# Optimization experiments

Hardware: AMD Instinct MI355X
Metric: run time of the kernel (lower is better)

The kernel has to match this reference:

```python
import jax, jax.numpy as jnp
import numpy as np

B, T, C, H = 4, 2048, 1024, 16
D = C // H  # head_dim = 64
ROPE_BASE = 10000.0
EPS = 1e-6


def _rms_norm(x):
    return x / jnp.sqrt(jnp.mean(x * x, axis=-1, keepdims=True) + EPS)


def _rope_tables(t_len, d, dtype):
    inv_freq = 1.0 / (ROPE_BASE ** (jnp.arange(0, d, 2, dtype=jnp.float32) / d))
    t = jnp.arange(t_len, dtype=jnp.float32)
    freqs = jnp.outer(t, inv_freq)  # [T, D/2]
    return jnp.cos(freqs).astype(dtype)[None, None], jnp.sin(freqs).astype(dtype)[None, None]


def _apply_rotary(x, cos, sin):
    d = x.shape[-1] // 2
    x1, x2 = x[..., :d], x[..., d:]
    return jnp.concatenate([x1 * cos + x2 * sin, -x1 * sin + x2 * cos], axis=-1)


def setup_inputs() -> dict:
    key = jax.random.key(0)
    k1, k2, k3, k4, k5 = jax.random.split(key, 5)
    x = jax.random.normal(k1, (B, T, C), dtype=jnp.float32)
    Wqkv = jax.random.normal(k2, (C, 3 * C), dtype=jnp.float32) * 0.02
    bqkv = jax.random.normal(k3, (3 * C,), dtype=jnp.float32) * 0.02
    # NOTE: original zero-inits c_proj.weight; randomized here for a non-trivial baseline.
    Wproj = jax.random.normal(k4, (C, C), dtype=jnp.float32) * 0.02
    bproj = jax.random.normal(k5, (C,), dtype=jnp.float32) * 0.02
    lamb = jnp.float32(0.5)
    return {"x": x, "Wqkv": Wqkv, "bqkv": bqkv, "Wproj": Wproj, "bproj": bproj, "lamb": lamb}


def reference(x, Wqkv, bqkv, Wproj, bproj, lamb):
    b, t, c = x.shape
    qkv = x @ Wqkv + bqkv  # [B,T,3C]
    q, k, v = jnp.split(qkv, 3, axis=-1)
    # [B,T,C] -> [B,H,T,D]
    to_heads = lambda z: z.reshape(b, t, H, D).transpose(0, 2, 1, 3)
    query, key_, value = to_heads(q), to_heads(k), to_heads(v)
    # v1 defaults to value -> blend is identity, kept for faithfulness
    value = (1.0 - lamb) * value + lamb * value
    query = _rms_norm(query)
    key_ = _rms_norm(key_)
    cos, sin = _rope_tables(t, D, x.dtype)
    query = _apply_rotary(query, cos, sin)
    key_ = _apply_rotary(key_, cos, sin)
    # causal SDPA
    scale = 1.0 / jnp.sqrt(jnp.float32(D)).astype(x.dtype)
    scores = jnp.einsum('bhqd,bhkd->bhqk', query, key_) * scale
    causal = jnp.tril(jnp.ones((t, t), dtype=bool))
    scores = jnp.where(causal[None, None], scores, jnp.finfo(scores.dtype).min)
    probs = jax.nn.softmax(scores, axis=-1)
    attn = jnp.einsum('bhqk,bhkd->bhqd', probs, value)
    attn = attn.transpose(0, 2, 1, 3).reshape(b, t, c)
    out = attn @ Wproj + bproj
    return out, value
```

## Files before the change

### kernel.cpp

```cpp
#include <hip/hip_runtime.h>
#include <math.h>

#define B_   4
#define T_   2048
#define C_   1024
#define H_   16
#define D_   64
#define TC3  3072

typedef __attribute__((ext_vector_type(8))) short short8;
typedef __attribute__((ext_vector_type(4))) short short4b;
typedef __attribute__((ext_vector_type(8))) unsigned short ushortv8;
typedef __attribute__((ext_vector_type(4))) float f32x4;
typedef __attribute__((ext_vector_type(4))) __bf16 bf16x4;

__device__ __forceinline__ float bf2f(unsigned short u) {
  unsigned int x = ((unsigned int)u) << 16;
  float f; __builtin_memcpy(&f, &x, 4); return f;
}
__device__ __forceinline__ unsigned short f2bf(float f) {
  unsigned int x; __builtin_memcpy(&x, &f, 4);
  x += 0x7fff + ((x >> 16) & 1);
  return (unsigned short)(x >> 16);
}

#define MFMA32(a, b, c) __builtin_amdgcn_mfma_f32_16x16x32_bf16(a, b, c, 0, 0, 0)
#if __has_builtin(__builtin_amdgcn_mfma_f32_16x16x16_bf16)
#define MFMA16(a, b, c) __builtin_amdgcn_mfma_f32_16x16x16_bf16(a, b, c, 0, 0, 0)
#else
#define MFMA16(a, b, c) __builtin_amdgcn_mfma_f32_16x16x16bf16_1k(a, b, c, 0, 0, 0)
#endif

#define GLOAD_LDS(gp, lp) __builtin_amdgcn_global_load_lds( \
    (const __attribute__((address_space(1))) unsigned int*)(gp), \
    (__attribute__((address_space(3))) unsigned int*)(lp), 16, 0, 0)

__global__ __launch_bounds__(256)
void convert_bf16(const float* __restrict__ x, unsigned short* __restrict__ xb) {
  const size_t i = ((size_t)blockIdx.x * 256 + threadIdx.x) * 8;
  float4 f0 = *(const float4*)(x + i);
  float4 f1 = *(const float4*)(x + i + 4);
  ushortv8 u = { f2bf(f0.x), f2bf(f0.y), f2bf(f0.z), f2bf(f0.w),
                 f2bf(f1.x), f2bf(f1.y), f2bf(f1.z), f2bf(f1.w) };
  *(ushortv8*)(xb + i) = u;
}

__global__ __launch_bounds__(256)
void transpose_bf16(const float* __restrict__ W, unsigned short* __restrict__ WT,
                    int K, int N) {
  __shared__ float tile[64][65];
  const int k0 = blockIdx.y * 64, n0 = blockIdx.x * 64;
  const int r = threadIdx.x >> 4, c4 = (threadIdx.x & 15) * 4;
#pragma unroll
  for (int p = 0; p < 4; ++p) {
    int kk = p * 16 + r;
    float4 v = *(const float4*)(W + (size_t)(k0 + kk) * N + n0 + c4);
    tile[kk][c4 + 0] = v.x; tile[kk][c4 + 1] = v.y;
    tile[kk][c4 + 2] = v.z; tile[kk][c4 + 3] = v.w;
  }
  __syncthreads();
#pragma unroll
  for (int p = 0; p < 4; ++p) {
    int nn = p * 16 + r;
    ushort4 o = { f2bf(tile[c4 + 0][nn]), f2bf(tile[c4 + 1][nn]),
                  f2bf(tile[c4 + 2][nn]), f2bf(tile[c4 + 3][nn]) };
    *(ushort4*)(WT + (size_t)(n0 + nn) * K + k0 + c4) = o;
  }
}

template<bool OUT_BF16>
__global__ __launch_bounds__(256)
void gemm_mfma(const unsigned short* __restrict__ Ab,
               const unsigned short* __restrict__ Bt,
               const float* __restrict__ bias, void* __restrict__ Cv,
               int K, int lda, int ldb, int ldc) {
  __shared__ unsigned short As[128 * 64];
  __shared__ unsigned short Bs[128 * 64];
  const int tid = threadIdx.x;
  const int l = tid & 63, w = tid >> 6;
  const int m0 = blockIdx.y * 128, n0 = blockIdx.x * 128;
  const int wm = (w & 1) * 64, wn = (w >> 1) * 64;
  const int fr = l & 15, g = l >> 4;

  f32x4 acc[4][4];
#pragma unroll
  for (int i = 0; i < 4; ++i)
#pragma unroll
    for (int j = 0; j < 4; ++j) acc[i][j] = (f32x4)0.f;

  const int gr = l >> 3;
  const int gc = (l & 7) ^ gr;

  for (int kt = 0; kt < K; kt += 64) {
    __syncthreads();
#pragma unroll
    for (int q = 0; q < 4; ++q) {
      int rr = (w * 4 + q) * 8 + gr;
      GLOAD_LDS(Ab + (size_t)(m0 + rr) * lda + kt + gc * 8,
                &As[(w * 4 + q) * 512]);
      GLOAD_LDS(Bt + (size_t)(n0 + rr) * ldb + kt + gc * 8,
                &Bs[(w * 4 + q) * 512]);
    }
    __syncthreads();

#pragma unroll
    for (int s = 0; s < 2; ++s) {
      const int cofs = (((s * 4 + g) ^ (fr & 7)) << 3);
      short8 a[4], b[4];
#pragma unroll
      for (int i = 0; i < 4; ++i)
        a[i] = *(const short8*)&As[(wm + i * 16 + fr) * 64 + cofs];
#pragma unroll
      for (int j = 0; j < 4; ++j)
        b[j] = *(const short8*)&Bs[(wn + j * 16 + fr) * 64 + cofs];
#pragma unroll
      for (int i = 0; i < 4; ++i)
#pragma unroll
        for (int j = 0; j < 4; ++j)
          acc[i][j] = MFMA32(a[i], b[j], acc[i][j]);
    }
  }

#pragma unroll
  for (int j = 0; j < 4; ++j) {
    const int n = n0 + wn + j * 16 + fr;
    const float bv = bias[n];
#pragma unroll
    for (int i = 0; i < 4; ++i) {
#pragma unroll
      for (int rg = 0; rg < 4; ++rg) {
        const int m = m0 + wm + i * 16 + g * 4 + rg;
        float v = acc[i][j][rg] + bv;
        if (OUT_BF16) ((unsigned short*)Cv)[(size_t)m * ldc + n] = f2bf(v);
        else          ((float*)Cv)[(size_t)m * ldc + n] = v;
      }
    }
  }
}

__global__ __launch_bounds__(256)
void rmsrope_kernel(unsigned short* __restrict__ qkv) {
  const int unit = blockIdx.x * 4 + (threadIdx.x >> 6);
  const int lane = threadIdx.x & 63;
  const int b = unit / (T_ * H_);
  const int rem = unit % (T_ * H_);
  const int t = rem / H_;
  const int h = rem % H_;
  const size_t base = (size_t)(b * T_ + t) * TC3;

  const int i = lane & 31;
  const float inv = __builtin_amdgcn_exp2f(-13.2877123795494f * (float)(2 * i)
                                           * (1.0f / 64.0f));
  const float ang = (float)t * inv;
  const float cs = cosf(ang);
  const float sn = sinf(ang);

  {
    const size_t idx = base + h * 64 + lane;
    float q = bf2f(qkv[idx]);
    float ss = q * q;
    ss += __shfl_xor(ss, 32); ss += __shfl_xor(ss, 16);
    ss += __shfl_xor(ss, 8);  ss += __shfl_xor(ss, 4);
    ss += __shfl_xor(ss, 2);  ss += __shfl_xor(ss, 1);
    float qn = q * (1.0f / sqrtf(ss * (1.0f / 64.0f) + 1e-6f));
    float part = __shfl_xor(qn, 32);
    float out = (lane < 32) ? (qn * cs + part * sn) : (qn * cs - part * sn);
    qkv[idx] = f2bf(out);
  }
  {
    const size_t idx = base + C_ + h * 64 + lane;
    float k = bf2f(qkv[idx]);
    float ss = k * k;
    ss += __shfl_xor(ss, 32); ss += __shfl_xor(ss, 16);
    ss += __shfl_xor(ss, 8);  ss += __shfl_xor(ss, 4);
    ss += __shfl_xor(ss, 2);  ss += __shfl_xor(ss, 1);
    float kn = k * (1.0f / sqrtf(ss * (1.0f / 64.0f) + 1e-6f));
    float part = __shfl_xor(kn, 32);
    float out = (lane < 32) ? (kn * cs + part * sn) : (kn * cs - part * sn);
    qkv[idx] = f2bf(out);
  }
}

__global__ __launch_bounds__(256)
void vtrans_kernel(const unsigned short* __restrict__ qkv,
                   const float* __restrict__ lambp,
                   unsigned short* __restrict__ vT,
                   float* __restrict__ valOut) {
  __shared__ float tile[64][65];
  const int t0 = blockIdx.x * 64;
  const int head = blockIdx.y;
  const int b = head >> 4, h = head & 15;
  const float lamb = lambp[0];
  const int r = threadIdx.x >> 4, c4 = (threadIdx.x & 15) * 4;
#pragma unroll
  for (int p = 0; p < 4; ++p) {
    int tt = p * 16 + r;
    ushort4 raw = *(const ushort4*)(
        qkv + (size_t)(b * T_ + t0 + tt) * TC3 + 2 * C_ + h * 64 + c4);
    float4 f;
    f.x = (1.f - lamb) * bf2f(raw.x) + lamb * bf2f(raw.x);
    f.y = (1.f - lamb) * bf2f(raw.y) + lamb * bf2f(raw.y);
    f.z = (1.f - lamb) * bf2f(raw.z) + lamb * bf2f(raw.z);
    f.w = (1.f - lamb) * bf2f(raw.w) + lamb * bf2f(raw.w);
    tile[tt][c4 + 0] = f.x; tile[tt][c4 + 1] = f.y;
    tile[tt][c4 + 2] = f.z; tile[tt][c4 + 3] = f.w;
    *(float4*)(valOut + ((size_t)head * T_ + t0 + tt) * D_ + c4) = f;
  }
  __syncthreads();
#pragma unroll
  for (int p = 0; p < 4; ++p) {
    int d = p * 16 + r;
    ushort4 o = { f2bf(tile[c4 + 0][d]), f2bf(tile[c4 + 1][d]),
                  f2bf(tile[c4 + 2][d]), f2bf(tile[c4 + 3][d]) };
    *(ushort4*)(vT + ((size_t)head * D_ + d) * T_ + t0 + c4) = o;
  }
}

#define SCL_ (0.125f * 1.44269504088896f)

#define PIPE_SYNC() do { \
  asm volatile("s_waitcnt vmcnt(0) lgkmcnt(0)" ::: "memory"); \
  __builtin_amdgcn_s_barrier(); \
  asm volatile("" ::: "memory"); \
} while (0)

__device__ __forceinline__ void attn_tile(
    const unsigned short* __restrict__ Ks,
    const unsigned short* __restrict__ Vs,
    const short8 (&qf)[2][2], int qrow0 , int k0,
    int fr, int quad, int f8,
    float (&l_pt)[2], f32x4 (&o)[2][4]) {
  f32x4 st[2][4];
#pragma unroll
  for (int i = 0; i < 2; ++i)
#pragma unroll
    for (int j = 0; j < 4; ++j) st[i][j] = (f32x4)0.f;

  __builtin_amdgcn_s_setprio(1);
#pragma unroll
  for (int kc = 0; kc < 2; ++kc) {
    const int cofs = (((kc * 4 + quad) ^ f8) << 3);
#pragma unroll
    for (int j = 0; j < 4; ++j) {
      short8 kf = *(const short8*)&Ks[(j * 16 + fr) * 64 + cofs];
      st[0][j] = MFMA32(kf, qf[kc][0], st[0][j]);
      st[1][j] = MFMA32(kf, qf[kc][1], st[1][j]);
    }
  }
  __builtin_amdgcn_s_setprio(0);

  short4b pa[2][4];
#pragma unroll
  for (int i = 0; i < 2; ++i) {
    const int qg = qrow0 + i * 16 + fr;
#pragma unroll
    for (int j = 0; j < 4; ++j) {
      const int kg = k0 + j * 16 + quad * 4;
#pragma unroll
      for (int r = 0; r < 4; ++r) {
        float arg = st[i][j][r] * SCL_;
        if (kg + r > qg) arg = -INFINITY;
        float p = __builtin_amdgcn_exp2f(arg);
        l_pt[i] += p;
        st[i][j][r] = p;
      }
      bf16x4 pb = { (__bf16)st[i][j][0], (__bf16)st[i][j][1],
                    (__bf16)st[i][j][2], (__bf16)st[i][j][3] };
      pa[i][j] = __builtin_bit_cast(short4b, pb);
    }
  }

  __builtin_amdgcn_s_setprio(1);
#pragma unroll
  for (int c = 0; c < 4; ++c) {
    const int vofs = ((((c * 2 + (quad >> 1)) ^ f8) << 3) + (quad & 1) * 4);
#pragma unroll
    for (int jd = 0; jd < 4; ++jd) {
      short4b vf = *(const short4b*)&Vs[(jd * 16 + fr) * 64 + vofs];
      o[0][jd] = MFMA16(pa[0][c], vf, o[0][jd]);
      o[1][jd] = MFMA16(pa[1][c], vf, o[1][jd]);
    }
  }
  __builtin_amdgcn_s_setprio(0);
}

__device__ __forceinline__ void attn_store(
    unsigned short* __restrict__ qkv, int bT, int h, int qrow0,
    int fr, int quad, float (&l_pt)[2], f32x4 (&o)[2][4]) {
#pragma unroll
  for (int i = 0; i < 2; ++i) {
    float lv = l_pt[i];
    lv += __shfl_xor(lv, 16);
    lv += __shfl_xor(lv, 32);
    float inv = 1.0f / lv;
    float invq[4];
#pragma unroll
    for (int r = 0; r < 4; ++r) invq[r] = __shfl(inv, quad * 4 + r);
#pragma unroll
    for (int jd = 0; jd < 4; ++jd) {
      const int d = jd * 16 + fr;
#pragma unroll
      for (int r = 0; r < 4; ++r) {
        const int row = qrow0 + i * 16 + quad * 4 + r;
        qkv[(size_t)(bT + row) * TC3 + 2 * C_ + h * 64 + d] =
            f2bf(o[i][jd][r] * invq[r]);
      }
    }
  }
}

__global__ __launch_bounds__(256)
void flash_mfma(unsigned short* __restrict__ qkv,
                const unsigned short* __restrict__ vT) {
  __shared__ unsigned short Ks0[64 * 64];
  __shared__ unsigned short Vs0[64 * 64];
  __shared__ unsigned short Ks1[64 * 64];
  __shared__ unsigned short Vs1[64 * 64];

  const int z = blockIdx.z;
  const int xx = ((int)blockIdx.x + ((z >> 1) << 3)) & 15;
  const int qt = (z & 1) ? (15 - xx) : xx;
  const int b  = z;
  const int h  = blockIdx.y;
  const int bT = b * T_;

  const int tid = threadIdx.x;
  const int w = tid >> 6, l = tid & 63;
  const int fr = l & 15, quad = l >> 4;
  const int q0 = qt * 128;
  const int gr = l >> 3;
  const int gc = (l & 7) ^ gr;
  const int f8 = fr & 7;

#define STAGE(KS, VS, KT) do { \
  const int _k0 = (KT) * 64; \
  _Pragma("unroll") \
  for (int s_ = 0; s_ < 2; ++s_) { \
    int row_ = w * 16 + s_ * 8; \
    GLOAD_LDS(qkv + (size_t)(bT + _k0 + row_ + gr) * TC3 + C_ + h * 64 + gc * 8, \
              &KS[row_ * 64]); \
    GLOAD_LDS(vT + ((size_t)(b * H_ + h) * D_ + row_ + gr) * T_ + _k0 + gc * 8, \
              &VS[row_ * 64]); \
  } \
} while (0)

#pragma unroll
  for (int s = 0; s < 4; ++s) {
    int rbase = w * 32 + s * 8;
    unsigned short* qdst = (rbase < 64) ? &Ks0[rbase * 64]
                                        : &Vs0[(rbase - 64) * 64];
    GLOAD_LDS(qkv + (size_t)(bT + q0 + rbase + gr) * TC3 + h * 64 + gc * 8, qdst);
  }
  STAGE(Ks1, Vs1, 0);
  __syncthreads();

  const unsigned short* Qb = (w < 2) ? Ks0 : Vs0;
  const int rq = (w < 2) ? w * 32 : (w - 2) * 32;
  short8 qf[2][2];
#pragma unroll
  for (int kc = 0; kc < 2; ++kc) {
    const int cofs = (((kc * 4 + quad) ^ f8) << 3);
    qf[kc][0] = *(const short8*)&Qb[(rq + fr) * 64 + cofs];
    qf[kc][1] = *(const short8*)&Qb[(rq + 16 + fr) * 64 + cofs];
  }
  __syncthreads();

  float l_pt[2] = {0.f, 0.f};
  f32x4 o[2][4];
#pragma unroll
  for (int i = 0; i < 2; ++i)
#pragma unroll
    for (int j = 0; j < 4; ++j) o[i][j] = (f32x4)0.f;

  const int nk = 2 * qt + 2;
  const int qr0 = q0 + w * 32;

  for (int kt = 0; kt < nk; kt += 2) {
    STAGE(Ks0, Vs0, kt + 1);
    attn_tile(Ks1, Vs1, qf, qr0, kt * 64, fr, quad, f8, l_pt, o);
    PIPE_SYNC();
    if (kt + 2 < nk) STAGE(Ks1, Vs1, kt + 2);
    attn_tile(Ks0, Vs0, qf, qr0, (kt + 1) * 64, fr, quad, f8, l_pt, o);
    if (kt + 2 < nk) PIPE_SYNC();
  }

  attn_store(qkv, bT, h, qr0, fr, quad, l_pt, o);
#undef STAGE
}

extern "C" void kernel_launch(void* const* d_in, const int* in_sizes, int n_in,
                              void* d_out, int out_size, void* d_ws, size_t ws_size,
                              hipStream_t stream) {
  const float* x     = (const float*)d_in[0];
  const float* Wqkv  = (const float*)d_in[1];
  const float* bqkv  = (const float*)d_in[2];
  const float* Wproj = (const float*)d_in[3];
  const float* bproj = (const float*)d_in[4];
  const float* lamb  = (const float*)d_in[5];

  float* out     = (float*)d_out;
  float* val_out = out + (size_t)B_ * T_ * C_;

  unsigned short* qkvb   = (unsigned short*)d_ws;
  unsigned short* WqkvT  = qkvb + (size_t)B_ * T_ * TC3;
  unsigned short* WprojT = WqkvT + (size_t)TC3 * C_;
  unsigned short* vT     = WprojT + (size_t)C_ * C_;
  unsigned short* xb     = vT + (size_t)B_ * H_ * D_ * T_;

  convert_bf16<<<dim3((B_ * T_ * C_) / 2048), 256, 0, stream>>>(x, xb);
  transpose_bf16<<<dim3(TC3 / 64, C_ / 64), 256, 0, stream>>>(Wqkv, WqkvT, C_, TC3);
  transpose_bf16<<<dim3(C_ / 64, C_ / 64), 256, 0, stream>>>(Wproj, WprojT, C_, C_);

  gemm_mfma<true><<<dim3(TC3 / 128, (B_ * T_) / 128), 256, 0, stream>>>(
      xb, WqkvT, bqkv, qkvb, C_, C_, C_, TC3);

  rmsrope_kernel<<<dim3((B_ * T_ * H_) / 4), 256, 0, stream>>>(qkvb);

  vtrans_kernel<<<dim3(T_ / 64, B_ * H_), 256, 0, stream>>>(qkvb, lamb, vT, val_out);

  flash_mfma<<<dim3(16, H_, B_), 256, 0, stream>>>(qkvb, vT);

  gemm_mfma<false><<<dim3(C_ / 128, (B_ * T_) / 128), 256, 0, stream>>>(
      qkvb + 2 * C_, WprojT, bproj, out, C_, TC3, C_, C_);
}
```

Baseline: 345.1 us.

## Restructure attention K/V double buffer with partial vmcnt waits per tile

Replaces the manually unrolled two-tile ping-pong loop with a single-tile loop over a 2x2 LDS buffer array. Each iteration issues the next tile's async global-to-LDS loads and then waits only until the current tile's loads have landed (vmcnt(4)), instead of a full vmcnt(0)+lgkmcnt(0) drain. The intent is to keep the next tile's loads in flight while computing the current tile. It adds two barriers per tile instead of one, and the correctness of the vmcnt count depends on exactly four outstanding loads per stage.

```diff
diff --git a/kernel.cpp b/kernel.cpp
--- a/kernel.cpp
+++ b/kernel.cpp
@@ -218,15 +218,9 @@
 
 #define SCL_ (0.125f * 1.44269504088896f)
 
-#define PIPE_SYNC() do { \
-  asm volatile("s_waitcnt vmcnt(0) lgkmcnt(0)" ::: "memory"); \
-  __builtin_amdgcn_s_barrier(); \
-  asm volatile("" ::: "memory"); \
-} while (0)
-
 __device__ __forceinline__ void attn_tile(
-    const unsigned short* __restrict__ Ks,
-    const unsigned short* __restrict__ Vs,
+    const unsigned short* Ks,
+    const unsigned short* Vs,
     const short8 (&qf)[2][2], int qrow0 , int k0,
     int fr, int quad, int f8,
     float (&l_pt)[2], f32x4 (&o)[2][4]) {
@@ -312,10 +306,7 @@
 __global__ __launch_bounds__(256)
 void flash_mfma(unsigned short* __restrict__ qkv,
                 const unsigned short* __restrict__ vT) {
-  __shared__ unsigned short Ks0[64 * 64];
-  __shared__ unsigned short Vs0[64 * 64];
-  __shared__ unsigned short Ks1[64 * 64];
-  __shared__ unsigned short Vs1[64 * 64];
+  __shared__ unsigned short KV[2][2][64 * 64];
 
   const int z = blockIdx.z;
   const int xx = ((int)blockIdx.x + ((z >> 1) << 3)) & 15;
@@ -338,30 +329,28 @@
   for (int s_ = 0; s_ < 2; ++s_) { \
     int row_ = w * 16 + s_ * 8; \
     GLOAD_LDS(qkv + (size_t)(bT + _k0 + row_ + gr) * TC3 + C_ + h * 64 + gc * 8, \
-              &KS[row_ * 64]); \
+              &(KS)[row_ * 64]); \
     GLOAD_LDS(vT + ((size_t)(b * H_ + h) * D_ + row_ + gr) * T_ + _k0 + gc * 8, \
-              &VS[row_ * 64]); \
+              &(VS)[row_ * 64]); \
   } \
 } while (0)
 
+  unsigned short* Qb = &KV[0][0][0];
 #pragma unroll
   for (int s = 0; s < 4; ++s) {
     int rbase = w * 32 + s * 8;
-    unsigned short* qdst = (rbase < 64) ? &Ks0[rbase * 64]
-                                        : &Vs0[(rbase - 64) * 64];
-    GLOAD_LDS(qkv + (size_t)(bT + q0 + rbase + gr) * TC3 + h * 64 + gc * 8, qdst);
-  }
-  STAGE(Ks1, Vs1, 0);
+    GLOAD_LDS(qkv + (size_t)(bT + q0 + rbase + gr) * TC3 + h * 64 + gc * 8,
+              Qb + rbase * 64);
+  }
+  STAGE(KV[1][0], KV[1][1], 0);
   __syncthreads();
 
-  const unsigned short* Qb = (w < 2) ? Ks0 : Vs0;
-  const int rq = (w < 2) ? w * 32 : (w - 2) * 32;
   short8 qf[2][2];
 #pragma unroll
   for (int kc = 0; kc < 2; ++kc) {
     const int cofs = (((kc * 4 + quad) ^ f8) << 3);
-    qf[kc][0] = *(const short8*)&Qb[(rq + fr) * 64 + cofs];
-    qf[kc][1] = *(const short8*)&Qb[(rq + 16 + fr) * 64 + cofs];
+    qf[kc][0] = *(const short8*)&Qb[(w * 32 + fr) * 64 + cofs];
+    qf[kc][1] = *(const short8*)&Qb[(w * 32 + 16 + fr) * 64 + cofs];
   }
   __syncthreads();
 
@@ -375,13 +364,26 @@
   const int nk = 2 * qt + 2;
   const int qr0 = q0 + w * 32;
 
-  for (int kt = 0; kt < nk; kt += 2) {
-    STAGE(Ks0, Vs0, kt + 1);
-    attn_tile(Ks1, Vs1, qf, qr0, kt * 64, fr, quad, f8, l_pt, o);
-    PIPE_SYNC();
-    if (kt + 2 < nk) STAGE(Ks1, Vs1, kt + 2);
-    attn_tile(Ks0, Vs0, qf, qr0, (kt + 1) * 64, fr, quad, f8, l_pt, o);
-    if (kt + 2 < nk) PIPE_SYNC();
+  int cur = 1;
+  for (int kt = 0; kt < nk; ++kt) {
+    const int nxt = cur ^ 1;
+    if (kt + 1 < nk) {
+      STAGE(KV[nxt][0], KV[nxt][1], kt + 1);
+      asm volatile("s_waitcnt vmcnt(4)" ::: "memory");
+    } else {
+      asm volatile("s_waitcnt vmcnt(0)" ::: "memory");
+    }
+    __builtin_amdgcn_s_barrier();
+    asm volatile("" ::: "memory");
+
+    attn_tile(&KV[cur][0][0], &KV[cur][1][0], qf, qr0, kt * 64,
+              fr, quad, f8, l_pt, o);
+
+    if (kt + 1 < nk) {
+      __builtin_amdgcn_s_barrier();
+      asm volatile("" ::: "memory");
+    }
+    cur = nxt;
   }
 
   attn_store(qkv, bT, h, qr0, fr, quad, l_pt, o);
```

New measurement: 326.5 us. 5.4% less time.
